# Kernel optimization log

Hardware: AMD Instinct MI355X
Metric: run time of the kernel (lower is better)

## Reference

```python
import jax, jax.numpy as jnp
import numpy as np

D = 1024
H = 16

def setup_inputs() -> dict:
    key = jax.random.key(0)
    ks = jax.random.split(key, 5)
    x = jax.random.normal(ks[0], (4, 2048, D), dtype=jnp.float32)
    lim = 1.0 / np.sqrt(D)
    W_qkv = jax.random.uniform(ks[1], (D, 3 * D), minval=-lim, maxval=lim, dtype=jnp.float32)
    b_qkv = jax.random.uniform(ks[2], (3 * D,), minval=-lim, maxval=lim, dtype=jnp.float32)
    W_proj = jax.random.uniform(ks[3], (D, D), minval=-lim, maxval=lim, dtype=jnp.float32)
    b_proj = jax.random.uniform(ks[4], (D,), minval=-lim, maxval=lim, dtype=jnp.float32)
    return {"x": x, "W_qkv": W_qkv, "b_qkv": b_qkv, "W_proj": W_proj, "b_proj": b_proj}

def reference(x, W_qkv, b_qkv, W_proj, b_proj):
    B, T, d = x.shape
    hd = d // H
    scale = hd ** (-0.5)
    qkv = x @ W_qkv + b_qkv                       # [B,T,3D]
    qkv = qkv.reshape(B, T, 3, H, hd)
    q = qkv[:, :, 0].transpose(0, 2, 1, 3)        # [B,H,T,hd]
    k = qkv[:, :, 1].transpose(0, 2, 1, 3)
    v = qkv[:, :, 2].transpose(0, 2, 1, 3)
    scores = jnp.einsum('bhqd,bhkd->bhqk', q, k) * scale
    attn = jax.nn.softmax(scores, axis=-1)
    y = jnp.einsum('bhqk,bhkd->bhqd', attn, v)    # [B,H,T,hd]
    y = y.transpose(0, 2, 1, 3).reshape(B, T, d)
    return y @ W_proj + b_proj
```

## Files before the change

kernel.cpp:

```cpp
#include <hip/hip_runtime.h>


typedef __attribute__((ext_vector_type(8))) short bf16x8;
typedef __attribute__((ext_vector_type(8))) unsigned short u16x8;
typedef __attribute__((ext_vector_type(4))) float f32x4;
typedef __attribute__((ext_vector_type(16))) float f32x16;

#define DEV static __device__ __forceinline__

DEV unsigned short f2b(float f) {
  union { float f; unsigned int i; } v; v.f = f;
  unsigned int x = v.i;
  return (unsigned short)((x + 0x7FFFu + ((x >> 16) & 1u)) >> 16);
}

DEV f32x4 mfma16(bf16x8 a, bf16x8 b, f32x4 c) {
  return __builtin_amdgcn_mfma_f32_16x16x32_bf16(a, b, c, 0, 0, 0);
}
DEV f32x16 mfma32(bf16x8 a, bf16x8 b, f32x16 c) {
  return __builtin_amdgcn_mfma_f32_32x32x16_bf16(a, b, c, 0, 0, 0);
}

DEV void gl_lds16(const unsigned short* g, unsigned short* l) {
  __builtin_amdgcn_global_load_lds(
      (const __attribute__((address_space(1))) unsigned int*)g,
      (__attribute__((address_space(3))) unsigned int*)l, 16, 0, 0);
}

DEV void pk_swap(float a0, float a1, float b0, float b1,
                 unsigned int& w_lo, unsigned int& w_hi) {
  unsigned int a, b;
  asm("v_cvt_pk_bf16_f32 %0, %1, %2" : "=v"(a) : "v"(a0), "v"(a1));
  asm("v_cvt_pk_bf16_f32 %0, %1, %2" : "=v"(b) : "v"(b0), "v"(b1));
  asm("v_permlane32_swap_b32 %0, %1" : "+v"(a), "+v"(b));
  w_lo = a; w_hi = b;
}

__global__ __launch_bounds__(256) void prep(
    const float* __restrict__ x, unsigned short* __restrict__ xbf,
    const float* __restrict__ Wqkv, unsigned short* __restrict__ WqkvT,
    const float* __restrict__ Wproj, unsigned short* __restrict__ WprojT) {
  const int bid = blockIdx.x;
  if (bid < 8192) {
    const int i = (bid * 256 + threadIdx.x) * 4;
    const float4 v = *(const float4*)(x + i);
    ushort4 o;
    o.x = f2b(v.x); o.y = f2b(v.y); o.z = f2b(v.z); o.w = f2b(v.w);
    *(ushort4*)(xbf + i) = o;
    return;
  }
  __shared__ float tile[32][33];
  const float* in; unsigned short* out; int C, bx, by;
  if (bid < 11264) {
    const int bb = bid - 8192;
    bx = bb % 96; by = bb / 96; in = Wqkv; out = WqkvT; C = 3072;
  } else {
    const int bb = bid - 11264;
    bx = bb % 32; by = bb / 32; in = Wproj; out = WprojT; C = 1024;
  }
  const int R = 1024;
  const int tx = threadIdx.x & 31, ty = threadIdx.x >> 5;
  const int c0 = bx * 32, r0 = by * 32;
#pragma unroll
  for (int i = 0; i < 32; i += 8)
    tile[ty + i][tx] = in[(size_t)(r0 + ty + i) * C + (c0 + tx)];
  __syncthreads();
#pragma unroll
  for (int i = 0; i < 32; i += 8)
    out[(size_t)(c0 + ty + i) * R + (r0 + tx)] = f2b(tile[tx][ty + i]);
}

#define QSCALE 0.18033688f
template <int MODE>
__global__ __launch_bounds__(256, 2) void gemm_bt(
    const unsigned short* __restrict__ A, const unsigned short* __restrict__ Bt,
    const float* __restrict__ bias, void* __restrict__ out_v,
    int M, int N, int K) {
  __shared__ __align__(16) unsigned short As[128 * 32];
  __shared__ __align__(16) unsigned short Bs[128 * 32];
  const int tid = threadIdx.x;
  const int w = tid >> 6, l = tid & 63, g = l >> 4, ln = l & 15;
  const int m0 = blockIdx.y * 128, n0 = blockIdx.x * 128;
  const int wm = (w & 1) * 64, wn = (w >> 1) * 64;

  f32x4 acc[4][4];
#pragma unroll
  for (int i = 0; i < 4; ++i)
#pragma unroll
    for (int j = 0; j < 4; ++j) acc[i][j] = (f32x4){0.f, 0.f, 0.f, 0.f};

  const unsigned short* Ab = A + (size_t)m0 * K;
  const unsigned short* Bb = Bt + (size_t)n0 * K;
  const int c0 = tid, c1 = tid + 256;
  const int ar0 = c0 >> 2, ar1 = c1 >> 2;
  const int ak0 = (((c0 & 3) ^ ((ar0 >> 1) & 3))) * 8;
  const int ak1 = (((c1 & 3) ^ ((ar1 >> 1) & 3))) * 8;
  const int xg = (g ^ ((ln >> 1) & 3)) * 8;

  for (int k0 = 0; k0 < K; k0 += 32) {
    gl_lds16(Ab + (size_t)ar0 * K + k0 + ak0, &As[c0 * 8]);
    gl_lds16(Ab + (size_t)ar1 * K + k0 + ak1, &As[c1 * 8]);
    gl_lds16(Bb + (size_t)ar0 * K + k0 + ak0, &Bs[c0 * 8]);
    gl_lds16(Bb + (size_t)ar1 * K + k0 + ak1, &Bs[c1 * 8]);
    __syncthreads();
    bf16x8 af[4], bf[4];
#pragma unroll
    for (int mi = 0; mi < 4; ++mi)
      af[mi] = *(const bf16x8*)&As[(wm + mi * 16 + ln) * 32 + xg];
#pragma unroll
    for (int ni = 0; ni < 4; ++ni)
      bf[ni] = *(const bf16x8*)&Bs[(wn + ni * 16 + ln) * 32 + xg];
#pragma unroll
    for (int mi = 0; mi < 4; ++mi)
#pragma unroll
      for (int ni = 0; ni < 4; ++ni)
        acc[mi][ni] = mfma16(af[mi], bf[ni], acc[mi][ni]);
    __syncthreads();
  }

#pragma unroll
  for (int mi = 0; mi < 4; ++mi) {
#pragma unroll
    for (int ni = 0; ni < 4; ++ni) {
      const int row0 = m0 + wm + mi * 16 + 4 * g;
      const int col = n0 + wn + ni * 16 + ln;
      const float bv = bias[col];
      if (MODE == 0) {
        const int which = col >> 10;
        const int h = (col >> 6) & 15;
        const int dd = col & 63;
        const int b = row0 >> 11, t0 = row0 & 2047;
        if (which == 2) {
          unsigned short* dst = (unsigned short*)out_v + (size_t)3 * 8388608u;
          ushort4 o;
          o.x = f2b(acc[mi][ni][0] + bv);
          o.y = f2b(acc[mi][ni][1] + bv);
          o.z = f2b(acc[mi][ni][2] + bv);
          o.w = f2b(acc[mi][ni][3] + bv);
          *(ushort4*)&dst[(((size_t)(b * 16 + h)) * 64 + dd) * 2048 + t0] = o;
        } else {
          unsigned short* dst = (unsigned short*)out_v + (size_t)which * 8388608u;
#pragma unroll
          for (int r = 0; r < 4; ++r) {
            float v = acc[mi][ni][r] + bv;
            if (which == 0) v *= QSCALE;
            dst[(((size_t)(b * 16 + h)) * 2048 + t0 + r) * 64 + dd] = f2b(v);
          }
        }
      } else {
#pragma unroll
        for (int r = 0; r < 4; ++r)
          ((float*)out_v)[(size_t)(row0 + r) * N + col] = acc[mi][ni][r] + bv;
      }
    }
  }
}

__global__ __launch_bounds__(256, 2) void attn(
    const unsigned short* __restrict__ Q, const unsigned short* __restrict__ K,
    const unsigned short* __restrict__ Vtg, unsigned short* __restrict__ Y) {
  __shared__ __align__(16) unsigned short Qs[128 * 72];
  __shared__ __align__(16) unsigned short Ks[64 * 72];
  __shared__ __align__(16) unsigned short Vt[64 * 72];

  const int tid = threadIdx.x;
  const int w = tid >> 6, l = tid & 63;
  const int l32 = l & 31, lh = l >> 5;
  const int wg = blockIdx.y * 16 + blockIdx.x;
  const int swz = (wg & 7) * 128 + (wg >> 3);
  const int bh = swz >> 4;
  const int q0 = (swz & 15) * 128;

  const unsigned short* Qb = Q + (size_t)bh * 131072;
  const unsigned short* Kb = K + (size_t)bh * 131072;
  const unsigned short* Vb = Vtg + (size_t)bh * 131072;

#pragma unroll
  for (int i = 0; i < 4; ++i) {
    const int c = tid + i * 256;
    u16x8 v = *(const u16x8*)(Qb + (size_t)q0 * 64 + c * 8);
    *(u16x8*)&Qs[(c >> 3) * 72 + (c & 7) * 8] = v;
  }
  __syncthreads();
  bf16x8 aq[4];
#pragma unroll
  for (int kb = 0; kb < 4; ++kb)
    aq[kb] = *(const bf16x8*)&Qs[(w * 32 + l32) * 72 + kb * 16 + lh * 8];

  const short one_b = (short)0x3F80;
  const bf16x8 vones = (bf16x8){one_b, one_b, one_b, one_b,
                                one_b, one_b, one_b, one_b};

  f32x16 o[2], os;
#pragma unroll
  for (int db = 0; db < 2; ++db)
#pragma unroll
    for (int r = 0; r < 16; ++r) o[db][r] = 0.f;
#pragma unroll
  for (int r = 0; r < 16; ++r) os[r] = 0.f;

  for (int kt = 0; kt < 32; ++kt) {
#pragma unroll
    for (int i = 0; i < 2; ++i) {
      const int c = tid + i * 256;
      const int row = c >> 3, cc = (c & 7) * 8;
      u16x8 kv = *(const u16x8*)(Kb + (size_t)kt * 4096 + c * 8);
      u16x8 vv = *(const u16x8*)(Vb + (size_t)row * 2048 + kt * 64 + cc);
      *(u16x8*)&Ks[row * 72 + cc] = kv;
      *(u16x8*)&Vt[row * 72 + cc] = vv;
    }
    __syncthreads();

    f32x16 s[2];
#pragma unroll
    for (int nb = 0; nb < 2; ++nb) {
#pragma unroll
      for (int r = 0; r < 16; ++r) s[nb][r] = 0.f;
#pragma unroll
      for (int kb = 0; kb < 4; ++kb) {
        bf16x8 bk = *(const bf16x8*)&Ks[(nb * 32 + l32) * 72 + kb * 16 + lh * 8];
        s[nb] = mfma32(bk, aq[kb], s[nb]);
      }
    }

    bf16x8 ap[4];
#pragma unroll
    for (int nb = 0; nb < 2; ++nb) {
      float pe[16];
#pragma unroll
      for (int r = 0; r < 16; ++r)
        pe[r] = __builtin_amdgcn_exp2f(s[nb][r]);
      union { unsigned int wd[4]; bf16x8 v; } u0, u1;
      pk_swap(pe[0], pe[1], pe[4], pe[5], u0.wd[0], u0.wd[2]);
      pk_swap(pe[2], pe[3], pe[6], pe[7], u0.wd[1], u0.wd[3]);
      pk_swap(pe[8], pe[9], pe[12], pe[13], u1.wd[0], u1.wd[2]);
      pk_swap(pe[10], pe[11], pe[14], pe[15], u1.wd[1], u1.wd[3]);
      ap[2 * nb + 0] = u0.v;
      ap[2 * nb + 1] = u1.v;
    }

#pragma unroll
    for (int ks = 0; ks < 4; ++ks) {
      os = mfma32(ap[ks], vones, os);
#pragma unroll
      for (int db = 0; db < 2; ++db) {
        bf16x8 bv = *(const bf16x8*)&Vt[(db * 32 + l32) * 72 + ks * 16 + lh * 8];
        o[db] = mfma32(ap[ks], bv, o[db]);
      }
    }
    __syncthreads();
  }

  float iv[16];
#pragma unroll
  for (int r = 0; r < 16; ++r) iv[r] = 1.f / os[r];

  const int b = bh >> 4, h = bh & 15;
#pragma unroll
  for (int db = 0; db < 2; ++db)
#pragma unroll
    for (int r = 0; r < 16; ++r) {
      const int row = (r & 3) + 8 * (r >> 2) + 4 * lh;
      const int t = q0 + w * 32 + row;
      Y[(size_t)(b * 2048 + t) * 1024 + h * 64 + db * 32 + l32] =
          f2b(o[db][r] * iv[r]);
    }
}

extern "C" void kernel_launch(void* const* d_in, const int* in_sizes, int n_in,
                              void* d_out, int out_size, void* d_ws, size_t ws_size,
                              hipStream_t stream) {
  const float* x     = (const float*)d_in[0];
  const float* Wqkv  = (const float*)d_in[1];
  const float* bqkv  = (const float*)d_in[2];
  const float* Wproj = (const float*)d_in[3];
  const float* bproj = (const float*)d_in[4];
  float* out = (float*)d_out;
  unsigned short* ws = (unsigned short*)d_ws;

  unsigned short* xbf    = ws;
  unsigned short* Yw     = xbf;
  unsigned short* WqkvT  = xbf + 8388608;
  unsigned short* WprojT = WqkvT + 3072 * 1024;
  unsigned short* Qw     = WprojT + 1024 * 1024;
  unsigned short* Kw     = Qw + 8388608;
  unsigned short* Vw     = Kw + 8388608;
  unsigned short* Vtw    = Vw + 8388608;
  (void)Vw;

  prep<<<12288, 256, 0, stream>>>(x, xbf, Wqkv, WqkvT, Wproj, WprojT);
  gemm_bt<0><<<dim3(24, 64), 256, 0, stream>>>(xbf, WqkvT, bqkv, Qw, 8192, 3072, 1024);
  attn<<<dim3(16, 64), 256, 0, stream>>>(Qw, Kw, Vtw, Yw);
  gemm_bt<1><<<dim3(8, 64), 256, 0, stream>>>(Yw, WprojT, bproj, out, 8192, 1024, 1024);
}
```

Before: 267.9 us.

## Double GEMM K-tile to 64 with 8-way XOR swizzle and remap workgroups

```diff
diff --git a/kernel.cpp b/kernel.cpp
--- a/kernel.cpp
+++ b/kernel.cpp
@@ -76,12 +76,16 @@
     const unsigned short* __restrict__ A, const unsigned short* __restrict__ Bt,
     const float* __restrict__ bias, void* __restrict__ out_v,
     int M, int N, int K) {
-  __shared__ __align__(16) unsigned short As[128 * 32];
-  __shared__ __align__(16) unsigned short Bs[128 * 32];
+  __shared__ __align__(16) unsigned short As[128 * 64];
+  __shared__ __align__(16) unsigned short Bs[128 * 64];
   const int tid = threadIdx.x;
   const int w = tid >> 6, l = tid & 63, g = l >> 4, ln = l & 15;
-  const int m0 = blockIdx.y * 128, n0 = blockIdx.x * 128;
   const int wm = (w & 1) * 64, wn = (w >> 1) * 64;
+
+  const int nwg = gridDim.x * gridDim.y;
+  int wg = blockIdx.y * gridDim.x + blockIdx.x;
+  wg = (wg & 7) * (nwg >> 3) + (wg >> 3);
+  const int m0 = (wg / gridDim.x) * 128, n0 = (wg % gridDim.x) * 128;
 
   f32x4 acc[4][4];
 #pragma unroll
@@ -91,30 +95,34 @@
 
   const unsigned short* Ab = A + (size_t)m0 * K;
   const unsigned short* Bb = Bt + (size_t)n0 * K;
-  const int c0 = tid, c1 = tid + 256;
-  const int ar0 = c0 >> 2, ar1 = c1 >> 2;
-  const int ak0 = (((c0 & 3) ^ ((ar0 >> 1) & 3))) * 8;
-  const int ak1 = (((c1 & 3) ^ ((ar1 >> 1) & 3))) * 8;
-  const int xg = (g ^ ((ln >> 1) & 3)) * 8;
-
-  for (int k0 = 0; k0 < K; k0 += 32) {
-    gl_lds16(Ab + (size_t)ar0 * K + k0 + ak0, &As[c0 * 8]);
-    gl_lds16(Ab + (size_t)ar1 * K + k0 + ak1, &As[c1 * 8]);
-    gl_lds16(Bb + (size_t)ar0 * K + k0 + ak0, &Bs[c0 * 8]);
-    gl_lds16(Bb + (size_t)ar1 * K + k0 + ak1, &Bs[c1 * 8]);
+  const int lx = ln & 7;
+
+  for (int k0 = 0; k0 < K; k0 += 64) {
+#pragma unroll
+    for (int i = 0; i < 4; ++i) {
+      const int ch = tid + i * 256;
+      const int ar = ch >> 3, s = ch & 7;
+      const int sc = (s ^ (ar & 7)) * 8;
+      gl_lds16(Ab + (size_t)ar * K + k0 + sc, &As[ch * 8]);
+      gl_lds16(Bb + (size_t)ar * K + k0 + sc, &Bs[ch * 8]);
+    }
     __syncthreads();
-    bf16x8 af[4], bf[4];
-#pragma unroll
-    for (int mi = 0; mi < 4; ++mi)
-      af[mi] = *(const bf16x8*)&As[(wm + mi * 16 + ln) * 32 + xg];
-#pragma unroll
-    for (int ni = 0; ni < 4; ++ni)
-      bf[ni] = *(const bf16x8*)&Bs[(wn + ni * 16 + ln) * 32 + xg];
-#pragma unroll
-    for (int mi = 0; mi < 4; ++mi)
+#pragma unroll
+    for (int ks = 0; ks < 2; ++ks) {
+      const int so = ((ks * 4 + g) ^ lx) * 8;
+      bf16x8 af[4], bf[4];
+#pragma unroll
+      for (int mi = 0; mi < 4; ++mi)
+        af[mi] = *(const bf16x8*)&As[(wm + mi * 16 + ln) * 64 + so];
 #pragma unroll
       for (int ni = 0; ni < 4; ++ni)
-        acc[mi][ni] = mfma16(af[mi], bf[ni], acc[mi][ni]);
+        bf[ni] = *(const bf16x8*)&Bs[(wn + ni * 16 + ln) * 64 + so];
+#pragma unroll
+      for (int mi = 0; mi < 4; ++mi)
+#pragma unroll
+        for (int ni = 0; ni < 4; ++ni)
+          acc[mi][ni] = mfma16(af[mi], bf[ni], acc[mi][ni]);
+    }
     __syncthreads();
   }
 
@@ -286,10 +294,10 @@
   unsigned short* Kw     = Qw + 8388608;
   unsigned short* Vw     = Kw + 8388608;
   unsigned short* Vtw    = Vw + 8388608;
-  (void)Vw;
+  (void)Vw; (void)Kw;
 
   prep<<<12288, 256, 0, stream>>>(x, xbf, Wqkv, WqkvT, Wproj, WprojT);
   gemm_bt<0><<<dim3(24, 64), 256, 0, stream>>>(xbf, WqkvT, bqkv, Qw, 8192, 3072, 1024);
-  attn<<<dim3(16, 64), 256, 0, stream>>>(Qw, Kw, Vtw, Yw);
+  attn<<<dim3(16, 64), 256, 0, stream>>>(Qw, Qw + 8388608, Vtw, Yw);
   gemm_bt<1><<<dim3(8, 64), 256, 0, stream>>>(Yw, WprojT, bproj, out, 8192, 1024, 1024);
 }
```

After: 253.0 us. 1.06x faster.
